# Kernel optimization log

Hardware: AMD Instinct MI355X
Metric: run time of the kernel (lower is better)

The kernel has to match this reference:

```python
import jax, jax.numpy as jnp
import numpy as np

N_OUT = 4096
N_IN = 4096
TOKENS = 8192
BITWIDTH = 4
GROUP_SIZE = 128
ZERO = 2 ** (BITWIDTH - 1)  # symmetric GPTQ zero-point


def setup_inputs() -> dict:
    key = jax.random.key(0)
    kx, kq, ks = jax.random.split(key, 3)
    x = jax.random.normal(kx, (TOKENS, N_IN), dtype=jnp.float32)
    qweight = jax.random.randint(kq, (N_OUT, N_IN), 0, 2 ** BITWIDTH, dtype=jnp.int32)
    scales = jax.random.uniform(ks, (N_OUT, N_IN // GROUP_SIZE), dtype=jnp.float32) * 0.02 + 0.001
    return {"x": x, "qweight": qweight, "scales": scales}


def reference(x, qweight, scales):
    # Dequantize: W[o, i] = (q[o, i] - zero) * scales[o, i // group_size]
    q = qweight.astype(x.dtype) - jnp.asarray(ZERO, dtype=x.dtype)
    # reshape input dim into (n_groups, group_size) and broadcast group scales
    qg = q.reshape(N_OUT, N_IN // GROUP_SIZE, GROUP_SIZE)
    w = (qg * scales[:, :, None].astype(x.dtype)).reshape(N_OUT, N_IN)
    # out = x @ W^T  -> [tokens, n_out]
    return jnp.einsum('ti,oi->to', x, w)
```

## Files before the change

kernel.cpp:

```cpp
#include <hip/hip_runtime.h>
#include <hip/hip_bf16.h>
#include <stdint.h>

#define TOKENS_C 8192
#define NIN_C    4096
#define NOUT_C   4096
#define GROUP_C  128
#define QZERO_C  8

typedef float   f32x4  __attribute__((ext_vector_type(4)));
typedef int     i32x4  __attribute__((ext_vector_type(4)));

#define GAS __attribute__((address_space(1)))
#define LAS __attribute__((address_space(3)))

__device__ __forceinline__ void gload16(const void* g, void* l) {
  __builtin_amdgcn_global_load_lds((const GAS void*)g, (LAS void*)l, 16, 0, 0);
}

__global__ __launch_bounds__(256) void quant_x_kernel(
    const float* __restrict__ x, char* __restrict__ x8, float* __restrict__ sx)
{
  const int t   = blockIdx.x;
  const int tid = threadIdx.x;
  const float* xr = x + (size_t)t * NIN_C;
  f32x4 v[4];
#pragma unroll
  for (int r = 0; r < 4; ++r) v[r] = *(const f32x4*)(xr + tid * 16 + r * 4);
  float m = 0.f;
#pragma unroll
  for (int r = 0; r < 4; ++r)
#pragma unroll
    for (int e = 0; e < 4; ++e) m = fmaxf(m, fabsf(v[r][e]));
#pragma unroll
  for (int off = 32; off >= 1; off >>= 1) m = fmaxf(m, __shfl_xor(m, off));
  __shared__ float wmax[4];
  if ((tid & 63) == 0) wmax[tid >> 6] = m;
  __syncthreads();
  m = fmaxf(fmaxf(wmax[0], wmax[1]), fmaxf(wmax[2], wmax[3]));
  m = fmaxf(m, 1e-20f);
  const float inv = 127.0f / m;
  if (tid == 0) sx[t] = m / 127.0f;
  i32x4 o;
#pragma unroll
  for (int r = 0; r < 4; ++r) {
    int q0 = (int)rintf(v[r][0] * inv), q1 = (int)rintf(v[r][1] * inv);
    int q2 = (int)rintf(v[r][2] * inv), q3 = (int)rintf(v[r][3] * inv);
    o[r] = (q0 & 255) | ((q1 & 255) << 8) | ((q2 & 255) << 16) | ((q3 & 255) << 24);
  }
  *(i32x4*)(x8 + (size_t)t * NIN_C + tid * 16) = o;
}

__global__ __launch_bounds__(256) void repack_w_kernel(
    const int* __restrict__ qw, char* __restrict__ w8)
{
  const size_t base = ((size_t)blockIdx.x * 256 + threadIdx.x) * 16;
  i32x4 o;
#pragma unroll
  for (int r = 0; r < 4; ++r) {
    i32x4 q = *(const i32x4*)(qw + base + r * 4);
    o[r] = ((q[0] - QZERO_C) & 255) | (((q[1] - QZERO_C) & 255) << 8) |
           (((q[2] - QZERO_C) & 255) << 16) | (((q[3] - QZERO_C) & 255) << 24);
  }
  *(i32x4*)(w8 + base) = o;
}

__global__ __launch_bounds__(256) void tsc_kernel(
    const float* __restrict__ sc, float* __restrict__ sT)
{
  const int id = blockIdx.x * 256 + threadIdx.x;
  const int o = id & (NOUT_C - 1), g = id >> 12;
  sT[id] = sc[o * (NIN_C / GROUP_C) + g];
}

#define BM 256
#define BN 256
#define BKB 64
#define NT (NIN_C / BKB)

__global__ __launch_bounds__(1024) void gemm_i8_kernel(
    const char* __restrict__ Ag,
    const char* __restrict__ Bg,
    const float* __restrict__ sTg,
    const float* __restrict__ sx,
    float* __restrict__ C)
{
  constexpr int N = NOUT_C, KB = NIN_C;
  __shared__ char smem[65536];

  const int tid  = threadIdx.x;
  const int lane = tid & 63;
  const int wid  = tid >> 6;
  const int wm   = wid >> 2;
  const int wn   = wid & 3;
  const int bm   = blockIdx.x;
  const int bn   = blockIdx.y;

  const int frow  = lane & 15;
  const int klane = lane >> 4;

  const int gsrc = ((tid & 3) ^ ((tid >> 3) & 3)) * 16;
  const uint32_t aoff = (uint32_t)((bm * BM + (tid >> 2)) * KB + gsrc);
  const uint32_t boff = (uint32_t)((bn * BN + (tid >> 2)) * KB + gsrc);
  const int sdst = tid * 16;

#define STG(tt, SW) { char* d_ = smem + (SW) * 32768 + sdst;                   \
    gload16(Ag + aoff + (uint32_t)(tt) * BKB, d_);                             \
    gload16(Bg + boff + (uint32_t)(tt) * BKB, d_ + 16384); }

  const int ccol0 = bn * BN + wn * 64;
  const int scoff = ccol0 + frow;
#define LD_S(dst, g)                                                           \
  _Pragma("unroll")                                                            \
  for (int j_ = 0; j_ < 4; ++j_)                                               \
    dst[j_] = sTg[(size_t)(g) * NOUT_C + scoff + j_ * 16];

  const int kswz = (klane ^ ((frow >> 1) & 3)) << 4;
  const int ard0 = (wm * 64 + frow) * 64 + kswz;
  const int brd0 = (wn * 64 + frow) * 64 + kswz + 16384;

  f32x4 facc[4][4] = {};
  const i32x4 zq = {0, 0, 0, 0};

#define MFI(a_, b_, c_) __builtin_amdgcn_mfma_i32_16x16x64_i8(a_, b_, c_, 0, 0, 0)
#define APPLY(ii, jj, pv, scur)                                                \
  { f32x4 tf_;                                                                 \
    tf_[0] = (float)(pv)[0]; tf_[1] = (float)(pv)[1];                          \
    tf_[2] = (float)(pv)[2]; tf_[3] = (float)(pv)[3];                          \
    facc[ii][jj] += tf_ * (scur)[jj]; }
#define BAR __builtin_amdgcn_s_barrier()
#define WAITV(n) asm volatile("s_waitcnt vmcnt(" #n ")" ::: "memory")
#define SBAR0 __builtin_amdgcn_sched_barrier(0)

#define TILE(tt, SLOT, scur, DO_LDS, snxt, gnxt, DO_STG)                       \
  {                                                                            \
    const char* As_ = smem + (SLOT) * 32768;                                   \
    const char* Bs_ = smem + (SLOT) * 32768;                                   \
    if (DO_LDS) { LD_S(snxt, gnxt); }                                          \
    if (DO_STG) { STG((tt) + 1, (SLOT) ^ 1); }                                 \
    i32x4 bf0 = *(const i32x4*)(Bs_ + brd0);                                   \
    i32x4 bf1 = *(const i32x4*)(Bs_ + brd0 + 1024);                            \
    i32x4 bf2 = *(const i32x4*)(Bs_ + brd0 + 2048);                            \
    i32x4 bf3 = *(const i32x4*)(Bs_ + brd0 + 3072);                            \
    _Pragma("unroll")                                                          \
    for (int ii = 0; ii < 4; ++ii) {                                           \
      i32x4 ak = *(const i32x4*)(As_ + ard0 + ii * 1024);                      \
      i32x4 p0, p1, p2, p3;                                                    \
      p0 = MFI(ak, bf0, zq); p1 = MFI(ak, bf1, zq);                            \
      p2 = MFI(ak, bf2, zq); p3 = MFI(ak, bf3, zq);                            \
      APPLY(ii, 0, p0, scur); APPLY(ii, 1, p1, scur);                          \
      APPLY(ii, 2, p2, scur); APPLY(ii, 3, p3, scur);                          \
    }                                                                          \
    WAITV(0); SBAR0; BAR;                                                      \
  }

  float sA[4], sB[4];

  LD_S(sA, 0);
  STG(0, 0);
  WAITV(0);
  BAR; SBAR0;

  for (int t0 = 0; t0 < 56; t0 += 4) {
    const int g0 = t0 >> 1;
    TILE(t0,     0, sA, 1, sB, g0 + 1, 1);
    TILE(t0 + 1, 1, sA, 0, sB, 0,      1);
    TILE(t0 + 2, 0, sB, 1, sA, g0 + 2, 1);
    TILE(t0 + 3, 1, sB, 0, sA, 0,      1);
  }
  TILE(56, 0, sA, 1, sB, 29, 1);
  TILE(57, 1, sA, 0, sB, 0,  1);
  TILE(58, 0, sB, 1, sA, 30, 1);
  TILE(59, 1, sB, 0, sA, 0,  1);
  TILE(60, 0, sA, 1, sB, 31, 1);
  TILE(61, 1, sA, 0, sB, 0,  1);
  TILE(62, 0, sB, 0, sA, 0,  1);
  TILE(63, 1, sB, 0, sA, 0,  0);

  const int crow0 = bm * BM + wm * 64;
  const int r0 = klane << 2;
  char* const wb = smem + wid * 4096;
#pragma unroll
  for (int fi = 0; fi < 4; ++fi) {
    const f32x4 sxv = *(const f32x4*)(sx + crow0 + fi * 16 + r0);
#pragma unroll
    for (int j = 0; j < 4; ++j) {
      f32x4 v = facc[fi][j];
#pragma unroll
      for (int r = 0; r < 4; ++r)
        *(float*)(wb + (r0 + r) * 256 + (j * 16 + frow) * 4) = v[r] * sxv[r];
    }
    __syncthreads();
#pragma unroll
    for (int sub = 0; sub < 4; ++sub) {
      const int row16 = klane + sub * 4;
      f32x4 v = *(const f32x4*)(wb + row16 * 256 + frow * 16);
      *(f32x4*)(C + (int64_t)(crow0 + fi * 16 + row16) * N + ccol0 + frow * 4) = v;
    }
    __syncthreads();
  }
#undef STG
#undef LD_S
#undef MFI
#undef APPLY
#undef TILE
#undef BAR
#undef WAITV
#undef SBAR0
}

__global__ __launch_bounds__(256) void naive_kernel(
    const float* __restrict__ x, const int* __restrict__ qw,
    const float* __restrict__ sc, float* __restrict__ out)
{
  const int64_t idx = (int64_t)blockIdx.x * 256 + threadIdx.x;
  const int tok = (int)(idx >> 12);
  const int o   = (int)(idx & 4095);
  const float* xr = x + (int64_t)tok * NIN_C;
  const int* qr = qw + (int64_t)o * NIN_C;
  float acc = 0.f;
  for (int g = 0; g < NIN_C / GROUP_C; ++g) {
    float s = sc[(o << 5) | g];
    float ga = 0.f;
#pragma unroll 4
    for (int i = g * GROUP_C; i < (g + 1) * GROUP_C; ++i)
      ga += xr[i] * (float)(qr[i] - QZERO_C);
    acc += s * ga;
  }
  out[idx] = acc;
}

extern "C" void kernel_launch(void* const* d_in, const int* in_sizes, int n_in,
                              void* d_out, int out_size, void* d_ws, size_t ws_size,
                              hipStream_t stream) {
  const float* x  = (const float*)d_in[0];
  const int*   qw = (const int*)d_in[1];
  const float* sc = (const float*)d_in[2];
  float* out = (float*)d_out;

  const size_t x8_bytes = (size_t)TOKENS_C * NIN_C;
  const size_t w8_bytes = (size_t)NOUT_C * NIN_C;
  const size_t sx_bytes = (size_t)TOKENS_C * sizeof(float);
  const size_t sT_bytes = (size_t)(NIN_C / GROUP_C) * NOUT_C * sizeof(float);

  if (ws_size < x8_bytes + w8_bytes + sx_bytes + sT_bytes) {
    const int64_t total = (int64_t)TOKENS_C * NOUT_C;
    naive_kernel<<<(int)(total / 256), 256, 0, stream>>>(x, qw, sc, out);
    return;
  }

  char*  x8 = (char*)d_ws;
  char*  w8 = (char*)d_ws + x8_bytes;
  float* sx = (float*)((char*)d_ws + x8_bytes + w8_bytes);
  float* sT = (float*)((char*)d_ws + x8_bytes + w8_bytes + sx_bytes);

  quant_x_kernel<<<TOKENS_C, 256, 0, stream>>>(x, x8, sx);
  repack_w_kernel<<<(int)(w8_bytes / 16 / 256), 256, 0, stream>>>(qw, w8);
  tsc_kernel<<<(int)((NIN_C / GROUP_C) * NOUT_C / 256), 256, 0, stream>>>(sc, sT);
  {
    dim3 grid(TOKENS_C / BM, NOUT_C / BN);
    gemm_i8_kernel<<<grid, 1024, 0, stream>>>(x8, w8, sT, sx, out);
  }
}
```

Measured before the change: 280.5 us.

## Switch GEMM to 256x128 tiles with 512 threads and triple-buffered LDS

Shrinks the output tile from 256x256 to 256x128 and the block from 1024 to 512 threads (8 waves in a 4x2 layout), with launch bounds asking for several blocks per CU. It replaces the double-buffered LDS pipeline with a three-slot ring that prefetches two tiles ahead and waits on a partial vmcnt instead of draining all loads each step. The goal is to hide global load latency and raise occupancy. In exchange there are more blocks, more total A-tile traffic, and a risk of register pressure from the occupancy target.

Result: slower. 332.2 us (+18.5%).

```diff
diff --git a/kernel.cpp b/kernel.cpp
--- a/kernel.cpp
+++ b/kernel.cpp
@@ -74,11 +74,12 @@
 }
 
 #define BM 256
-#define BN 256
+#define BN 128
 #define BKB 64
 #define NT (NIN_C / BKB)
-
-__global__ __launch_bounds__(1024) void gemm_i8_kernel(
+#define SLOT_SZ 24576
+
+__global__ __launch_bounds__(512, 4) void gemm_i8_kernel(
     const char* __restrict__ Ag,
     const char* __restrict__ Bg,
     const float* __restrict__ sTg,
@@ -86,13 +87,13 @@
     float* __restrict__ C)
 {
   constexpr int N = NOUT_C, KB = NIN_C;
-  __shared__ char smem[65536];
+  __shared__ char smem[3 * SLOT_SZ];
 
   const int tid  = threadIdx.x;
   const int lane = tid & 63;
   const int wid  = tid >> 6;
-  const int wm   = wid >> 2;
-  const int wn   = wid & 3;
+  const int wm   = wid >> 1;
+  const int wn   = wid & 1;
   const int bm   = blockIdx.x;
   const int bn   = blockIdx.y;
 
@@ -100,13 +101,15 @@
   const int klane = lane >> 4;
 
   const int gsrc = ((tid & 3) ^ ((tid >> 3) & 3)) * 16;
-  const uint32_t aoff = (uint32_t)((bm * BM + (tid >> 2)) * KB + gsrc);
-  const uint32_t boff = (uint32_t)((bn * BN + (tid >> 2)) * KB + gsrc);
+  const uint32_t aoff0 = (uint32_t)((bm * BM + (tid >> 2)) * KB + gsrc);
+  const uint32_t aoff1 = (uint32_t)((bm * BM + 128 + (tid >> 2)) * KB + gsrc);
+  const uint32_t boff  = (uint32_t)((bn * BN + (tid >> 2)) * KB + gsrc);
   const int sdst = tid * 16;
 
-#define STG(tt, SW) { char* d_ = smem + (SW) * 32768 + sdst;                   \
-    gload16(Ag + aoff + (uint32_t)(tt) * BKB, d_);                             \
-    gload16(Bg + boff + (uint32_t)(tt) * BKB, d_ + 16384); }
+#define STG(tt, SW) { char* d_ = smem + (SW) * SLOT_SZ + sdst;                 \
+    gload16(Ag + aoff0 + (uint32_t)(tt) * BKB, d_);                            \
+    gload16(Ag + aoff1 + (uint32_t)(tt) * BKB, d_ + 8192);                     \
+    gload16(Bg + boff  + (uint32_t)(tt) * BKB, d_ + 16384); }
 
   const int ccol0 = bn * BN + wn * 64;
   const int scoff = ccol0 + frow;
@@ -117,7 +120,7 @@
 
   const int kswz = (klane ^ ((frow >> 1) & 3)) << 4;
   const int ard0 = (wm * 64 + frow) * 64 + kswz;
-  const int brd0 = (wn * 64 + frow) * 64 + kswz + 16384;
+  const int brd0 = 16384 + (wn * 64 + frow) * 64 + kswz;
 
   f32x4 facc[4][4] = {};
   const i32x4 zq = {0, 0, 0, 0};
@@ -132,16 +135,15 @@
 #define WAITV(n) asm volatile("s_waitcnt vmcnt(" #n ")" ::: "memory")
 #define SBAR0 __builtin_amdgcn_sched_barrier(0)
 
-#define TILE(tt, SLOT, scur, DO_LDS, snxt, gnxt, DO_STG)                       \
+#define TILE(tt, SLOT, scur, DO_LDS, snxt, gnxt, DO_STG, WVN)                  \
   {                                                                            \
-    const char* As_ = smem + (SLOT) * 32768;                                   \
-    const char* Bs_ = smem + (SLOT) * 32768;                                   \
+    const char* As_ = smem + (SLOT) * SLOT_SZ;                                 \
     if (DO_LDS) { LD_S(snxt, gnxt); }                                          \
-    if (DO_STG) { STG((tt) + 1, (SLOT) ^ 1); }                                 \
-    i32x4 bf0 = *(const i32x4*)(Bs_ + brd0);                                   \
-    i32x4 bf1 = *(const i32x4*)(Bs_ + brd0 + 1024);                            \
-    i32x4 bf2 = *(const i32x4*)(Bs_ + brd0 + 2048);                            \
-    i32x4 bf3 = *(const i32x4*)(Bs_ + brd0 + 3072);                            \
+    if (DO_STG) { STG((tt) + 2, ((tt) + 2) % 3); }                             \
+    i32x4 bf0 = *(const i32x4*)(As_ + brd0);                                   \
+    i32x4 bf1 = *(const i32x4*)(As_ + brd0 + 1024);                            \
+    i32x4 bf2 = *(const i32x4*)(As_ + brd0 + 2048);                            \
+    i32x4 bf3 = *(const i32x4*)(As_ + brd0 + 3072);                            \
     _Pragma("unroll")                                                          \
     for (int ii = 0; ii < 4; ++ii) {                                           \
       i32x4 ak = *(const i32x4*)(As_ + ard0 + ii * 1024);                      \
@@ -151,31 +153,36 @@
       APPLY(ii, 0, p0, scur); APPLY(ii, 1, p1, scur);                          \
       APPLY(ii, 2, p2, scur); APPLY(ii, 3, p3, scur);                          \
     }                                                                          \
-    WAITV(0); SBAR0; BAR;                                                      \
+    WAITV(WVN); SBAR0; BAR;                                                    \
   }
 
   float sA[4], sB[4];
 
   LD_S(sA, 0);
-  STG(0, 0);
-  WAITV(0);
+  SBAR0;
+  STG(0, 0); STG(1, 1);
+  WAITV(3);
   BAR; SBAR0;
 
-  for (int t0 = 0; t0 < 56; t0 += 4) {
+  for (int t0 = 0; t0 < 60; t0 += 12) {
     const int g0 = t0 >> 1;
-    TILE(t0,     0, sA, 1, sB, g0 + 1, 1);
-    TILE(t0 + 1, 1, sA, 0, sB, 0,      1);
-    TILE(t0 + 2, 0, sB, 1, sA, g0 + 2, 1);
-    TILE(t0 + 3, 1, sB, 0, sA, 0,      1);
-  }
-  TILE(56, 0, sA, 1, sB, 29, 1);
-  TILE(57, 1, sA, 0, sB, 0,  1);
-  TILE(58, 0, sB, 1, sA, 30, 1);
-  TILE(59, 1, sB, 0, sA, 0,  1);
-  TILE(60, 0, sA, 1, sB, 31, 1);
-  TILE(61, 1, sA, 0, sB, 0,  1);
-  TILE(62, 0, sB, 0, sA, 0,  1);
-  TILE(63, 1, sB, 0, sA, 0,  0);
+    TILE(t0 + 0,  0, sA, 1, sB, g0 + 1, 1, 3);
+    TILE(t0 + 1,  1, sA, 0, sB, 0,      1, 3);
+    TILE(t0 + 2,  2, sB, 1, sA, g0 + 2, 1, 3);
+    TILE(t0 + 3,  0, sB, 0, sA, 0,      1, 3);
+    TILE(t0 + 4,  1, sA, 1, sB, g0 + 3, 1, 3);
+    TILE(t0 + 5,  2, sA, 0, sB, 0,      1, 3);
+    TILE(t0 + 6,  0, sB, 1, sA, g0 + 4, 1, 3);
+    TILE(t0 + 7,  1, sB, 0, sA, 0,      1, 3);
+    TILE(t0 + 8,  2, sA, 1, sB, g0 + 5, 1, 3);
+    TILE(t0 + 9,  0, sA, 0, sB, 0,      1, 3);
+    TILE(t0 + 10, 1, sB, 1, sA, g0 + 6, 1, 3);
+    TILE(t0 + 11, 2, sB, 0, sA, 0,      1, 3);
+  }
+  TILE(60, 0, sA, 1, sB, 31, 1, 3);
+  TILE(61, 1, sA, 0, sB, 0,  1, 3);
+  TILE(62, 2, sB, 0, sA, 0,  0, 0);
+  TILE(63, 0, sB, 0, sA, 0,  0, 0);
 
   const int crow0 = bm * BM + wm * 64;
   const int r0 = klane << 2;
@@ -259,6 +266,6 @@
   tsc_kernel<<<(int)((NIN_C / GROUP_C) * NOUT_C / 256), 256, 0, stream>>>(sc, sT);
   {
     dim3 grid(TOKENS_C / BM, NOUT_C / BN);
-    gemm_i8_kernel<<<grid, 1024, 0, stream>>>(x8, w8, sT, sx, out);
-  }
-}
+    gemm_i8_kernel<<<grid, 512, 0, stream>>>(x8, w8, sT, sx, out);
+  }
+}
```
